# Optimization experiments

Hardware: AMD Instinct MI355X
Metric: run time of the kernel (lower is better)

Reference implementation:

```python
import jax, jax.numpy as jnp
import numpy as np

B, L, LQ = 64, 4096, 128
D = 32        # input_dim (value channels)
ET = 128      # embed_time
NH = 1        # num_heads
H = 128       # nhidden
NC = 6        # n_classes


def _time_emb(tt, lin_w, lin_b, per_w, per_b):
    # tt [..., T] -> [..., T, ET]; cat(Linear(1,1)(t), sin(Linear(1,ET-1)(t)))
    tt = tt[..., None]
    out1 = tt * lin_w[0, 0] + lin_b
    out2 = jnp.sin(tt @ per_w + per_b)
    return jnp.concatenate([out1, out2], axis=-1)


def _gru_dir(xs, wih, whh, bih, bhh, reverse):
    # xs [B, T, I] -> [B, T, H]; torch GRU gate math
    xs_t = jnp.swapaxes(xs, 0, 1)              # [T, B, I]
    if reverse:
        xs_t = xs_t[::-1]
    gi_all = xs_t @ wih.T + bih                # [T, B, 3H] precomputed input gates
    h0 = jnp.zeros((xs.shape[0], H), xs.dtype)

    def step(h, gi):
        gh = h @ whh.T + bhh
        ir, iz, inn = jnp.split(gi, 3, axis=-1)
        hr, hz, hn = jnp.split(gh, 3, axis=-1)
        r = jax.nn.sigmoid(ir + hr)
        z = jax.nn.sigmoid(iz + hz)
        n = jnp.tanh(inn + r * hn)
        h_new = (1.0 - z) * n + z * h
        return h_new, h_new

    _, ys = jax.lax.scan(step, h0, gi_all)     # [T, B, H]
    if reverse:
        ys = ys[::-1]
    return jnp.swapaxes(ys, 0, 1)


def _bigru(xs, wih, whh, bih, bhh):
    fwd = _gru_dir(xs, wih[0], whh[0], bih[0], bhh[0], False)
    bwd = _gru_dir(xs, wih[1], whh[1], bih[1], bhh[1], True)
    return jnp.concatenate([fwd, bwd], axis=-1)


def setup_inputs() -> dict:
    ks = jax.random.split(jax.random.key(0), 32)
    w = lambda i, s: jax.random.normal(ks[i], s, jnp.float32) * 0.05
    G3 = 3 * H
    return {
        "x": jax.random.normal(ks[0], (B, L, D), jnp.float32),
        "time_steps": jax.random.uniform(ks[1], (B, L), dtype=jnp.float32),
        "query_times": jnp.linspace(0.0, 1.0, LQ, dtype=jnp.float32),
        "lin_w": w(2, (1, 1)), "lin_b": w(3, (1,)),
        "per_w": w(4, (1, ET - 1)), "per_b": w(5, (ET - 1,)),
        "wq": w(6, (ET, ET)), "bq": w(7, (ET,)),
        "wk": w(8, (ET, ET)), "bk": w(9, (ET,)),
        "wo": w(10, (NH * D, H)), "bo": w(11, (H,)),
        "gru0_wih": w(12, (2, G3, H)), "gru0_whh": w(13, (2, G3, H)),
        "gru0_bih": w(14, (2, G3)), "gru0_bhh": w(15, (2, G3)),
        "gru1_wih": w(16, (2, G3, 2 * H)), "gru1_whh": w(17, (2, G3, H)),
        "gru1_bih": w(18, (2, G3)), "gru1_bhh": w(19, (2, G3)),
        "c1_w": w(20, (2 * H, 128)), "c1_b": w(21, (128,)),
        "c2_w": w(22, (128, 64)), "c2_b": w(23, (64,)),
        "c3_w": w(24, (64, NC)), "c3_b": w(25, (NC,)),
    }


def reference(x, time_steps, query_times, lin_w, lin_b, per_w, per_b,
              wq, bq, wk, bk, wo, bo,
              gru0_wih, gru0_whh, gru0_bih, gru0_bhh,
              gru1_wih, gru1_whh, gru1_bih, gru1_bhh,
              c1_w, c1_b, c2_w, c2_b, c3_w, c3_b):
    ek = ET // NH
    # learned time embeddings
    q = _time_emb(query_times[None, :], lin_w, lin_b, per_w, per_b)  # [1, LQ, ET]
    k = _time_emb(time_steps, lin_w, lin_b, per_w, per_b)            # [B, L, ET]
    # per-head projections
    qp = (q @ wq + bq).reshape(1, LQ, NH, ek).transpose(0, 2, 1, 3)[0]  # [NH, LQ, ek]
    kp = (k @ wk + bk).reshape(B, L, NH, ek).transpose(0, 2, 1, 3)      # [B, NH, L, ek]
    # mTAN attention: scores are channel-independent (mask=None), so the
    # per-channel repeat+softmax reduces to a single softmax over keys.
    scores = jnp.einsum('hqe,bhke->bhqk', qp, kp) / jnp.sqrt(jnp.float32(ek))
    p = jax.nn.softmax(scores, axis=-1)                                 # [B, NH, LQ, L]
    att = jnp.einsum('bhqk,bkd->bqhd', p, x).reshape(B, LQ, NH * D)
    att_out = att @ wo + bo                                             # [B, LQ, H]
    # 2-layer bidirectional GRU
    g0 = _bigru(att_out, gru0_wih, gru0_whh, gru0_bih, gru0_bhh)        # [B, LQ, 2H]
    g1 = _bigru(g0, gru1_wih, gru1_whh, gru1_bih, gru1_bhh)             # [B, LQ, 2H]
    class_in = jnp.concatenate([g1[:, -1, :H], g1[:, 0, H:]], axis=1)   # [B, 2H]
    out = ((class_in @ c1_w + c1_b) @ c2_w + c2_b) @ c3_w + c3_b        # [B, NC]
    return out
```

## Files before the change

### kernel.cpp

```cpp
#include <hip/hip_runtime.h>
#include <math.h>

#define Bn   64
#define Ln   4096
#define LQn  128
#define Dn   32
#define ETn  128
#define Hn   128
#define G3n  384
#define NDEG 12

typedef __attribute__((ext_vector_type(2))) float f32x2;

#define DPPF(x, ctrl) __int_as_float(__builtin_amdgcn_update_dpp(0, __float_as_int(x), (ctrl), 0xF, 0xF, true))
#define QP_XOR1 0xB1
#define QP_XOR2 0x4E
#define QP_B0   0x00
#define QP_B1   0x55
#define QP_B2   0xAA
#define QP_B3   0xFF

__device__ __forceinline__ float sin_poly(float x) {
    const float x2 = x * x;
    float r = -1.9841270114e-04f;
    r = fmaf(r, x2,  8.3333337680e-03f);
    r = fmaf(r, x2, -1.6666667163e-01f);
    return fmaf(r * x2, x, x);
}
__device__ __forceinline__ float cos_poly(float x) {
    const float x2 = x * x;
    float r =  2.4801587642e-05f;
    r = fmaf(r, x2, -1.3888888899e-03f);
    r = fmaf(r, x2,  4.1666667908e-02f);
    r = fmaf(r, x2, -5.0000000000e-01f);
    return fmaf(r, x2, 1.0f);
}

#define WS_C    0
#define WS_WT   4096
#define WS_B2   (WS_WT + 768*32)
#define WS_CLS  (WS_B2 + 1024)
#define WS_G0   (WS_CLS + Bn*2*Hn)
#define WS_GI   (WS_G0 + Bn*LQn*2*Hn)
#define WS_ACCP WS_G0
#define WS_SP   (WS_G0 + 1048576)

__global__ __launch_bounds__(128) void k_coef(
    const float* __restrict__ qtimes, const float* __restrict__ lin_w,
    const float* __restrict__ lin_b, const float* __restrict__ per_w,
    const float* __restrict__ per_b, const float* __restrict__ wq,
    const float* __restrict__ bq, const float* __restrict__ wk,
    const float* __restrict__ bk, float* __restrict__ C)
{
    __shared__ float qe[ETn], qp_l[ETn], qt_l[ETn], bas[NDEG * 128], red[96], qbk_red[32];
    const int q = blockIdx.x, tid = threadIdx.x;
    if (tid < ETn - 1) {
        const float w = per_w[tid], bb = per_b[tid];
        const float sb = sin_poly(bb), cb = cos_poly(bb);
        float wp = 1.f;
#pragma unroll
        for (int d = 0; d < NDEG; ++d) {
            const float sd = ((d & 3) == 0) ? sb : ((d & 3) == 1) ? cb : ((d & 3) == 2) ? -sb : -cb;
            bas[d * 128 + tid] = wp * sd;
            wp *= w / (float)(d + 1);
        }
    }
    const float t = qtimes[q];
    qe[tid] = (tid == 0) ? fmaf(t, lin_w[0], lin_b[0])
                         : sin_poly(fmaf(t, per_w[tid - 1], per_b[tid - 1]));
    __syncthreads();
    {
        float a = bq[tid];
#pragma unroll 16
        for (int i = 0; i < ETn; ++i) a = fmaf(qe[i], wq[i * ETn + tid], a);
        qp_l[tid] = a;
    }
    __syncthreads();
    {
        const float4* wk4 = (const float4*)(wk + (size_t)tid * ETn);
        const float4* qp4 = (const float4*)qp_l;
        float a = 0.f;
#pragma unroll
        for (int k = 0; k < 32; ++k) {
            const float4 w4 = wk4[k], p4 = qp4[k];
            a += w4.x * p4.x + w4.y * p4.y + w4.z * p4.z + w4.w * p4.w;
        }
        qt_l[tid] = a;
    }
    __syncthreads();
    if (tid < 96) {
        const int d = tid >> 3, g = tid & 7;
        float p = 0.f;
        for (int j = g; j < ETn - 1; j += 8) p = fmaf(qt_l[j + 1], bas[d * 128 + j], p);
        red[tid] = p;
    } else {
        const int g2 = tid - 96;
        float p = 0.f;
#pragma unroll
        for (int k = 0; k < 4; ++k) p = fmaf(qp_l[g2 + 32 * k], bk[g2 + 32 * k], p);
        qbk_red[g2] = p;
    }
    __syncthreads();
    if (tid < NDEG) {
        const int d = tid;
        float s = red[d * 8 + 0] + red[d * 8 + 1] + red[d * 8 + 2] + red[d * 8 + 3]
                + red[d * 8 + 4] + red[d * 8 + 5] + red[d * 8 + 6] + red[d * 8 + 7];
        if (d == 0) {
            float qbk = 0.f;
#pragma unroll
            for (int k = 0; k < 32; ++k) qbk += qbk_red[k];
            s += qt_l[0] * lin_b[0] + qbk;
        }
        if (d == 1) s += qt_l[0] * lin_w[0];
        C[q * NDEG + d] = s * 0.08838834764831845f;
    }
}

__global__ __launch_bounds__(256) void k_fuse(
    const float* __restrict__ wih, const float* __restrict__ wo,
    const float* __restrict__ bo, const float* __restrict__ bih,
    float* __restrict__ Wt, float* __restrict__ bias2)
{
    const int t = blockIdx.x * 256 + threadIdx.x;
    if (t < 768 * 32) {
        const int o = t >> 5, d = t & 31;
        const float4* wr4 = (const float4*)(wih + (size_t)o * 128);
        const float4* wc4 = (const float4*)(wo + (size_t)d * 128);
        float a = 0.f;
#pragma unroll
        for (int k = 0; k < 32; ++k) {
            const float4 r4 = wr4[k], c4 = wc4[k];
            a += r4.x * c4.x + r4.y * c4.y + r4.z * c4.z + r4.w * c4.w;
        }
        Wt[t] = a;
    } else if (t < 768 * 33) {
        const int o = t - 768 * 32;
        const float4* wr4 = (const float4*)(wih + (size_t)o * 128);
        const float4* bo4 = (const float4*)bo;
        float a = bih[o];
#pragma unroll
        for (int k = 0; k < 32; ++k) {
            const float4 r4 = wr4[k], b4 = bo4[k];
            a += r4.x * b4.x + r4.y * b4.y + r4.z * b4.z + r4.w * b4.w;
        }
        bias2[o] = a;
    }
}

__global__ __launch_bounds__(512, 1) void k_attn(
    const float* __restrict__ x, const float* __restrict__ tsteps,
    const float* __restrict__ Cc, float* __restrict__ accP, float* __restrict__ sP)
{
    __shared__ float4 xls[4 * 64 * 8];
    __shared__ float  slab[4][128][36];
    const int tid = threadIdx.x;
    const int b = blockIdx.x >> 2, lsplit = blockIdx.x & 3;
    const int i = tid & 3, qt = (tid >> 2) & 31, ls2 = tid >> 7;
    const int qown = 4 * qt + i;
    const int u = tid & 127;

    float c[NDEG];
#pragma unroll
    for (int d = 0; d < NDEG; ++d) c[d] = Cc[qown * NDEG + d];

    const int l0 = lsplit * 1024 + ls2 * 256;
    const float4* tg4 = (const float4*)(tsteps + (size_t)b * Ln + l0);
    const float4* xg  = (const float4*)(x + ((size_t)b * Ln + l0) * Dn);

    f32x2 acc2[4][4];
#pragma unroll
    for (int m = 0; m < 4; ++m)
#pragma unroll
        for (int e = 0; e < 4; ++e) { acc2[m][e].x = 0.f; acc2[m][e].y = 0.f; }
    float s_own = 0.f;

    float4 xr[4];
#pragma unroll
    for (int w = 0; w < 4; ++w) xr[w] = xg[u + 128 * w];

    for (int ch = 0; ch < 4; ++ch) {
        __syncthreads();
#pragma unroll
        for (int w = 0; w < 4; ++w) xls[ls2 * 512 + u + 128 * w] = xr[w];
        __syncthreads();
        if (ch < 3) {
            const int off = (ch + 1) * 512;
#pragma unroll
            for (int w = 0; w < 4; ++w) xr[w] = xg[off + u + 128 * w];
        }
        const float4* xrow = &xls[ls2 * 512];
        for (int k = 0; k < 16; ++k) {
            const float4 t4 = tg4[ch * 16 + k];
#pragma unroll
            for (int jj = 0; jj < 4; ++jj) {
                const float t = (jj == 0) ? t4.x : (jj == 1) ? t4.y : (jj == 2) ? t4.z : t4.w;
                float sc = c[NDEG - 1];
#pragma unroll
                for (int d = NDEG - 2; d >= 0; --d) sc = fmaf(sc, t, c[d]);
                const float pe = __expf(sc);
                s_own += pe;
                const float p0 = DPPF(pe, QP_B0);
                const float p1 = DPPF(pe, QP_B1);
                const float p2 = DPPF(pe, QP_B2);
                const float p3 = DPPF(pe, QP_B3);
                const int lrow = (k * 4 + jj) * 8;
                const float4 xa = xrow[lrow + 2 * i];
                const float4 xb = xrow[lrow + 2 * i + 1];
                f32x2 xa0; xa0.x = xa.x; xa0.y = xa.y;
                f32x2 xa1; xa1.x = xa.z; xa1.y = xa.w;
                f32x2 xb0; xb0.x = xb.x; xb0.y = xb.y;
                f32x2 xb1; xb1.x = xb.z; xb1.y = xb.w;
#define PKA(m, pv) { f32x2 pp; pp.x = (pv); pp.y = (pv); \
    acc2[m][0] = __builtin_elementwise_fma(pp, xa0, acc2[m][0]); \
    acc2[m][1] = __builtin_elementwise_fma(pp, xa1, acc2[m][1]); \
    acc2[m][2] = __builtin_elementwise_fma(pp, xb0, acc2[m][2]); \
    acc2[m][3] = __builtin_elementwise_fma(pp, xb1, acc2[m][3]); }
                PKA(0, p0) PKA(1, p1) PKA(2, p2) PKA(3, p3)
#undef PKA
            }
        }
    }
    __syncthreads();
#pragma unroll
    for (int m = 0; m < 4; ++m) {
        float4 f4a, f4b;
        f4a.x = acc2[m][0].x; f4a.y = acc2[m][0].y; f4a.z = acc2[m][1].x; f4a.w = acc2[m][1].y;
        f4b.x = acc2[m][2].x; f4b.y = acc2[m][2].y; f4b.z = acc2[m][3].x; f4b.w = acc2[m][3].y;
        *(float4*)&slab[ls2][4 * qt + m][8 * i]     = f4a;
        *(float4*)&slab[ls2][4 * qt + m][8 * i + 4] = f4b;
    }
    slab[ls2][qown][32] = s_own;
    __syncthreads();
    const int q = tid & 127, part = tid >> 7;
#pragma unroll
    for (int j = 0; j < 2; ++j) {
        const int off = (part * 2 + j) * 4;
        float4 r  = *(float4*)&slab[0][q][off];
        float4 r1 = *(float4*)&slab[1][q][off];
        float4 r2 = *(float4*)&slab[2][q][off];
        float4 r3 = *(float4*)&slab[3][q][off];
        r.x += r1.x + r2.x + r3.x; r.y += r1.y + r2.y + r3.y;
        r.z += r1.z + r2.z + r3.z; r.w += r1.w + r2.w + r3.w;
        *(float4*)&accP[((((size_t)lsplit * Bn + b) * LQn + q) * 32) + off] = r;
    }
    if (part == 0) {
        sP[((size_t)lsplit * Bn + b) * LQn + q] =
            slab[0][q][32] + slab[1][q][32] + slab[2][q][32] + slab[3][q][32];
    }
}

__global__ __launch_bounds__(256) void k_gemm_att(
    const float* __restrict__ accP, const float* __restrict__ sP,
    const float* __restrict__ Bm, const float* __restrict__ bias,
    float* __restrict__ Cm)
{
    __shared__ float4 A_l[64 * 8];
    __shared__ float4 B_l[64 * 8];
    const int tid = threadIdx.x;
    const int m0 = blockIdx.x * 64, n0 = blockIdx.y * 64;
    const int r0 = (tid >> 4) << 2, c0 = (tid & 15) << 2;
    f32x2 acc2[4][4];
#pragma unroll
    for (int a = 0; a < 4; ++a)
#pragma unroll
        for (int bb = 0; bb < 4; ++bb) { acc2[a][bb].x = 0.f; acc2[a][bb].y = 0.f; }
    const float4* Ag = (const float4*)accP;
    const float4* Bg = (const float4*)Bm;

#pragma unroll
    for (int w = 0; w < 2; ++w) {
        const int idx = tid + w * 256;
        const int row = idx >> 3, c4 = idx & 7;
        const int sc = (c4 + row + (row >> 2)) & 7;
        const int m = m0 + row;
        float4 a0 = Ag[(size_t)m * 8 + c4];
        float4 a1 = Ag[((size_t)8192  + m) * 8 + c4];
        float4 a2 = Ag[((size_t)16384 + m) * 8 + c4];
        float4 a3 = Ag[((size_t)24576 + m) * 8 + c4];
        const float inv = 1.f / (sP[m] + sP[8192 + m] + sP[16384 + m] + sP[24576 + m]);
        float4 av;
        av.x = (a0.x + a1.x + a2.x + a3.x) * inv;
        av.y = (a0.y + a1.y + a2.y + a3.y) * inv;
        av.z = (a0.z + a1.z + a2.z + a3.z) * inv;
        av.w = (a0.w + a1.w + a2.w + a3.w) * inv;
        A_l[row * 8 + sc] = av;
        B_l[row * 8 + sc] = Bg[(size_t)(n0 + row) * 8 + c4];
    }
    __syncthreads();
#pragma unroll
    for (int k4 = 0; k4 < 8; ++k4) {
        float4 av[4], bv[4];
#pragma unroll
        for (int j = 0; j < 4; ++j) {
            const int ra = r0 + j;
            av[j] = A_l[ra * 8 + ((k4 + ra + (ra >> 2)) & 7)];
        }
#pragma unroll
        for (int j = 0; j < 4; ++j) {
            const int rb = c0 + j;
            bv[j] = B_l[rb * 8 + ((k4 + rb + (rb >> 2)) & 7)];
        }
#pragma unroll
        for (int ri = 0; ri < 4; ++ri) {
            f32x2 alo; alo.x = av[ri].x; alo.y = av[ri].y;
            f32x2 ahi; ahi.x = av[ri].z; ahi.y = av[ri].w;
#pragma unroll
            for (int ci = 0; ci < 4; ++ci) {
                f32x2 blo; blo.x = bv[ci].x; blo.y = bv[ci].y;
                f32x2 bhi; bhi.x = bv[ci].z; bhi.y = bv[ci].w;
                acc2[ri][ci] = __builtin_elementwise_fma(alo, blo, acc2[ri][ci]);
                acc2[ri][ci] = __builtin_elementwise_fma(ahi, bhi, acc2[ri][ci]);
            }
        }
    }
#pragma unroll
    for (int ri = 0; ri < 4; ++ri) {
        float4 o4;
        o4.x = acc2[ri][0].x + acc2[ri][0].y + bias[n0 + c0 + 0];
        o4.y = acc2[ri][1].x + acc2[ri][1].y + bias[n0 + c0 + 1];
        o4.z = acc2[ri][2].x + acc2[ri][2].y + bias[n0 + c0 + 2];
        o4.w = acc2[ri][3].x + acc2[ri][3].y + bias[n0 + c0 + 3];
        *(float4*)&Cm[(size_t)(m0 + r0 + ri) * 768 + n0 + c0] = o4;
    }
}

__global__ __launch_bounds__(256) void k_gemm_nt(
    const float* __restrict__ A, const float* __restrict__ Bm,
    const float* __restrict__ bias, float* __restrict__ Cm,
    int N, int K)
{
    __shared__ float4 A_l[64 * 8];
    __shared__ float4 B_l[64 * 8];
    const int tid = threadIdx.x;
    const int m0 = blockIdx.x * 64, n0 = blockIdx.y * 64;
    const int r0 = (tid >> 4) << 2, c0 = (tid & 15) << 2;
    const int K4 = K >> 2;
    f32x2 acc2[4][4];
#pragma unroll
    for (int a = 0; a < 4; ++a)
#pragma unroll
        for (int bb = 0; bb < 4; ++bb) { acc2[a][bb].x = 0.f; acc2[a][bb].y = 0.f; }
    const float4* Ag = (const float4*)A;
    const float4* Bg = (const float4*)Bm;

    for (int k0 = 0; k0 < K4; k0 += 8) {
        __syncthreads();
#pragma unroll
        for (int w = 0; w < 2; ++w) {
            const int idx = tid + w * 256;
            const int row = idx >> 3, c4 = idx & 7;
            const int sc = (c4 + row + (row >> 2)) & 7;
            A_l[row * 8 + sc] = Ag[(size_t)(m0 + row) * K4 + k0 + c4];
            B_l[row * 8 + sc] = Bg[(size_t)(n0 + row) * K4 + k0 + c4];
        }
        __syncthreads();
#pragma unroll
        for (int k4 = 0; k4 < 8; ++k4) {
            float4 av[4], bv[4];
#pragma unroll
            for (int j = 0; j < 4; ++j) {
                const int ra = r0 + j;
                av[j] = A_l[ra * 8 + ((k4 + ra + (ra >> 2)) & 7)];
            }
#pragma unroll
            for (int j = 0; j < 4; ++j) {
                const int rb = c0 + j;
                bv[j] = B_l[rb * 8 + ((k4 + rb + (rb >> 2)) & 7)];
            }
#pragma unroll
            for (int ri = 0; ri < 4; ++ri) {
                f32x2 alo; alo.x = av[ri].x; alo.y = av[ri].y;
                f32x2 ahi; ahi.x = av[ri].z; ahi.y = av[ri].w;
#pragma unroll
                for (int ci = 0; ci < 4; ++ci) {
                    f32x2 blo; blo.x = bv[ci].x; blo.y = bv[ci].y;
                    f32x2 bhi; bhi.x = bv[ci].z; bhi.y = bv[ci].w;
                    acc2[ri][ci] = __builtin_elementwise_fma(alo, blo, acc2[ri][ci]);
                    acc2[ri][ci] = __builtin_elementwise_fma(ahi, bhi, acc2[ri][ci]);
                }
            }
        }
    }
#pragma unroll
    for (int ri = 0; ri < 4; ++ri) {
        float4 o4;
        o4.x = acc2[ri][0].x + acc2[ri][0].y + bias[n0 + c0 + 0];
        o4.y = acc2[ri][1].x + acc2[ri][1].y + bias[n0 + c0 + 1];
        o4.z = acc2[ri][2].x + acc2[ri][2].y + bias[n0 + c0 + 2];
        o4.w = acc2[ri][3].x + acc2[ri][3].y + bias[n0 + c0 + 3];
        *(float4*)&Cm[(size_t)(m0 + r0 + ri) * N + n0 + c0] = o4;
    }
}

__global__ __launch_bounds__(256, 1) void k_gru(
    const float* __restrict__ gi, const float* __restrict__ whh,
    const float* __restrict__ bhh, float* __restrict__ seq_out,
    float* __restrict__ final_out)
{
    __shared__ float h_l[2][Hn];
    const int tid = threadIdx.x;
    const int b = blockIdx.x >> 1, dir = blockIdx.x & 1;
    const int j = tid >> 1, q = tid & 1;

    f32x2 wr[32], wz[32], wn[32];
    {
        const float* wb = whh + ((size_t)dir * G3n + j) * Hn + 64 * q;
        const f32x2* p0 = (const f32x2*)(wb);
        const f32x2* p1 = (const f32x2*)(wb + (size_t)128 * Hn);
        const f32x2* p2 = (const f32x2*)(wb + (size_t)256 * Hn);
#pragma unroll
        for (int k = 0; k < 32; ++k) { wr[k] = p0[k]; wz[k] = p1[k]; wn[k] = p2[k]; }
    }
    const float bhr = bhh[dir * G3n + j];
    const float bhz = bhh[dir * G3n + 128 + j];
    const float bhn = bhh[dir * G3n + 256 + j];

    if (tid < Hn) { h_l[0][tid] = 0.f; h_l[1][tid] = 0.f; }
    __syncthreads();

    const long sstride = dir ? -768 : 768;
    const float* gptr = gi + (size_t)b * LQn * 768 + dir * G3n + j
                        + (size_t)(dir ? LQn - 1 : 0) * 768;

    int cur = 0;
    float hlast = 0.f;

    auto gstep = [&](const float gir, const float giz, const float gin,
                     const int step) {
        const float hold = h_l[cur][j];
        const float4* hb = (const float4*)(&h_l[cur][q * 64]);
        f32x2 ar = {0.f, 0.f}, az = {0.f, 0.f}, an = {0.f, 0.f};
        f32x2 br = {0.f, 0.f}, bz = {0.f, 0.f}, bn = {0.f, 0.f};
#pragma unroll
        for (int cc = 0; cc < 16; ++cc) {
            float4 hv = hb[cc];
            f32x2 h01; h01.x = hv.x; h01.y = hv.y;
            f32x2 h23; h23.x = hv.z; h23.y = hv.w;
            asm("v_pk_fma_f32 %0, %1, %2, %0" : "+v"(ar) : "v"(wr[2 * cc]),     "v"(h01));
            asm("v_pk_fma_f32 %0, %1, %2, %0" : "+v"(az) : "v"(wz[2 * cc]),     "v"(h01));
            asm("v_pk_fma_f32 %0, %1, %2, %0" : "+v"(an) : "v"(wn[2 * cc]),     "v"(h01));
            asm("v_pk_fma_f32 %0, %1, %2, %0" : "+v"(br) : "v"(wr[2 * cc + 1]), "v"(h23));
            asm("v_pk_fma_f32 %0, %1, %2, %0" : "+v"(bz) : "v"(wz[2 * cc + 1]), "v"(h23));
            asm("v_pk_fma_f32 %0, %1, %2, %0" : "+v"(bn) : "v"(wn[2 * cc + 1]), "v"(h23));
        }
        float sr = (ar.x + br.x) + (ar.y + br.y);
        float sz = (az.x + bz.x) + (az.y + bz.y);
        float sn = (an.x + bn.x) + (an.y + bn.y);
        sr += DPPF(sr, QP_XOR1);
        sz += DPPF(sz, QP_XOR1);
        sn += DPPF(sn, QP_XOR1);
        const float r = 1.f / (1.f + __expf(-(gir + sr + bhr)));
        const float z = 1.f / (1.f + __expf(-(giz + sz + bhz)));
        const float nx = gin + r * (sn + bhn);
        const float n = 1.f - 2.f / (1.f + __expf(2.f * nx));
        const float hn = n + z * (hold - n);
        if (q == 0) {
            h_l[cur ^ 1][j] = hn;
            if (seq_out) {
                const int l = dir ? (LQn - 1 - step) : step;
                seq_out[((size_t)(b * LQn + l)) * (2 * Hn) + dir * Hn + j] = hn;
            }
        }
        hlast = hn;
        cur ^= 1;
        __syncthreads();
    };

    float gA[3], gB[3], gC[3], gD[3];
#define GLD(dst, s) { const long o = (long)(s) * sstride; \
    dst[0] = gptr[o]; dst[1] = gptr[o + 128]; dst[2] = gptr[o + 256]; }
    GLD(gA, 0) GLD(gB, 1) GLD(gC, 2) GLD(gD, 3)
    for (int s0 = 0; s0 < LQn; s0 += 4) {
        gstep(gA[0], gA[1], gA[2], s0);
        { const int sn2 = (s0 + 4 < LQn) ? s0 + 4 : LQn - 1; GLD(gA, sn2) }
        gstep(gB[0], gB[1], gB[2], s0 + 1);
        { const int sn2 = (s0 + 5 < LQn) ? s0 + 5 : LQn - 1; GLD(gB, sn2) }
        gstep(gC[0], gC[1], gC[2], s0 + 2);
        { const int sn2 = (s0 + 6 < LQn) ? s0 + 6 : LQn - 1; GLD(gC, sn2) }
        gstep(gD[0], gD[1], gD[2], s0 + 3);
        { const int sn2 = (s0 + 7 < LQn) ? s0 + 7 : LQn - 1; GLD(gD, sn2) }
    }
#undef GLD
    if (final_out && q == 0) final_out[b * 2 * Hn + dir * Hn + j] = hlast;
}

__global__ __launch_bounds__(256) void k_cls(
    const float* __restrict__ cls_in,
    const float* __restrict__ c1w, const float* __restrict__ c1b,
    const float* __restrict__ c2w, const float* __restrict__ c2b,
    const float* __restrict__ c3w, const float* __restrict__ c3b,
    float* __restrict__ out)
{
    __shared__ float ci[256], y1[128], y2[64];
    const int b = blockIdx.x, tid = threadIdx.x;
    ci[tid] = cls_in[b * 256 + tid];
    __syncthreads();
    if (tid < 128) { float a = c1b[tid]; for (int i = 0; i < 256; ++i) a += ci[i] * c1w[i * 128 + tid]; y1[tid] = a; }
    __syncthreads();
    if (tid < 64)  { float a = c2b[tid]; for (int i = 0; i < 128; ++i) a += y1[i] * c2w[i * 64 + tid];  y2[tid] = a; }
    __syncthreads();
    if (tid < 6)   { float a = c3b[tid]; for (int i = 0; i < 64; ++i)  a += y2[i] * c3w[i * 6 + tid];   out[b * 6 + tid] = a; }
}

extern "C" void kernel_launch(void* const* d_in, const int* in_sizes, int n_in,
                              void* d_out, int out_size, void* d_ws, size_t ws_size,
                              hipStream_t stream)
{
    const float* x        = (const float*)d_in[0];
    const float* tsteps   = (const float*)d_in[1];
    const float* qtimes   = (const float*)d_in[2];
    const float* lin_w    = (const float*)d_in[3];
    const float* lin_b    = (const float*)d_in[4];
    const float* per_w    = (const float*)d_in[5];
    const float* per_b    = (const float*)d_in[6];
    const float* wq       = (const float*)d_in[7];
    const float* bq       = (const float*)d_in[8];
    const float* wk       = (const float*)d_in[9];
    const float* bk       = (const float*)d_in[10];
    const float* wo       = (const float*)d_in[11];
    const float* bo       = (const float*)d_in[12];
    const float* g0_wih   = (const float*)d_in[13];
    const float* g0_whh   = (const float*)d_in[14];
    const float* g0_bih   = (const float*)d_in[15];
    const float* g0_bhh   = (const float*)d_in[16];
    const float* g1_wih   = (const float*)d_in[17];
    const float* g1_whh   = (const float*)d_in[18];
    const float* g1_bih   = (const float*)d_in[19];
    const float* g1_bhh   = (const float*)d_in[20];
    const float* c1w      = (const float*)d_in[21];
    const float* c1b      = (const float*)d_in[22];
    const float* c2w      = (const float*)d_in[23];
    const float* c2b      = (const float*)d_in[24];
    const float* c3w      = (const float*)d_in[25];
    const float* c3b      = (const float*)d_in[26];
    float* out = (float*)d_out;
    float* ws  = (float*)d_ws;

    float* Cws   = ws + WS_C;
    float* Wt    = ws + WS_WT;
    float* bias2 = ws + WS_B2;
    float* clsin = ws + WS_CLS;
    float* g0buf = ws + WS_G0;
    float* accP  = ws + WS_ACCP;
    float* sPb   = ws + WS_SP;
    float* gibuf = ws + WS_GI;

    k_coef<<<128, 128, 0, stream>>>(qtimes, lin_w, lin_b, per_w, per_b, wq, bq, wk, bk, Cws);
    k_fuse<<<99, 256, 0, stream>>>(g0_wih, wo, bo, g0_bih, Wt, bias2);
    k_attn<<<256, 512, 0, stream>>>(x, tsteps, Cws, accP, sPb);

    k_gemm_att<<<dim3(128, 12), 256, 0, stream>>>(accP, sPb, Wt, bias2, gibuf);
    k_gru<<<128, 256, 0, stream>>>(gibuf, g0_whh, g0_bhh, g0buf, nullptr);

    k_gemm_nt<<<dim3(128, 12), 256, 0, stream>>>(g0buf, g1_wih, g1_bih, gibuf, 768, 256);
    k_gru<<<128, 256, 0, stream>>>(gibuf, g1_whh, g1_bhh, nullptr, clsin);

    k_cls<<<64, 256, 0, stream>>>(clsin, c1w, c1b, c2w, c2b, c3w, c3b, out);
}
```

Measured before the change: 325.2 us.

## Use fp16 dot2 recurrent matvec in GRU with 4 lanes per hidden unit

The GRU recurrent weights are converted to fp16 and kept in registers, and the hidden state is mirrored in fp16 in shared memory so that v_dot2_f32_f16 can replace packed fp32 FMAs. The block doubles to 512 threads with 4 lanes per hidden unit, which halves the per-thread dot length and uses a two-stage DPP reduction. Each lane loads one of the three input-gate values, and these are spread across the quad with DPP broadcasts. This targets the serial per-step latency of the recurrence. The cost is reduced precision in the recurrent matvec, which can accumulate over 128 steps, plus a larger barrier across 8 waves.

```diff
diff --git a/kernel.cpp b/kernel.cpp
--- a/kernel.cpp
+++ b/kernel.cpp
@@ -11,6 +11,7 @@
 #define NDEG 12
 
 typedef __attribute__((ext_vector_type(2))) float f32x2;
+typedef __attribute__((ext_vector_type(2))) _Float16 f16x2;
 
 #define DPPF(x, ctrl) __int_as_float(__builtin_amdgcn_update_dpp(0, __float_as_int(x), (ctrl), 0xF, 0xF, true))
 #define QP_XOR1 0xB1
@@ -392,96 +393,117 @@
     }
 }
 
-__global__ __launch_bounds__(256, 1) void k_gru(
+__global__ __launch_bounds__(512) void k_gru(
     const float* __restrict__ gi, const float* __restrict__ whh,
     const float* __restrict__ bhh, float* __restrict__ seq_out,
     float* __restrict__ final_out)
 {
-    __shared__ float h_l[2][Hn];
+    __shared__ _Float16 h16[2][Hn];
+    __shared__ float    h32[2][Hn];
     const int tid = threadIdx.x;
     const int b = blockIdx.x >> 1, dir = blockIdx.x & 1;
-    const int j = tid >> 1, q = tid & 1;
-
-    f32x2 wr[32], wz[32], wn[32];
+    const int j = tid >> 2, q = tid & 3;
+
+    f16x2 wr[16], wz[16], wn[16];
     {
-        const float* wb = whh + ((size_t)dir * G3n + j) * Hn + 64 * q;
+        const float* wb = whh + ((size_t)dir * G3n + j) * Hn + 32 * q;
         const f32x2* p0 = (const f32x2*)(wb);
         const f32x2* p1 = (const f32x2*)(wb + (size_t)128 * Hn);
         const f32x2* p2 = (const f32x2*)(wb + (size_t)256 * Hn);
 #pragma unroll
-        for (int k = 0; k < 32; ++k) { wr[k] = p0[k]; wz[k] = p1[k]; wn[k] = p2[k]; }
+        for (int k = 0; k < 16; ++k) {
+            f32x2 a = p0[k], bz2 = p1[k], c2 = p2[k];
+            wr[k].x = (_Float16)a.x;   wr[k].y = (_Float16)a.y;
+            wz[k].x = (_Float16)bz2.x; wz[k].y = (_Float16)bz2.y;
+            wn[k].x = (_Float16)c2.x;  wn[k].y = (_Float16)c2.y;
+        }
+    }
+#pragma unroll
+    for (int k = 0; k < 16; ++k) {
+        asm volatile("" : "+v"(wr[k]));
+        asm volatile("" : "+v"(wz[k]));
+        asm volatile("" : "+v"(wn[k]));
     }
     const float bhr = bhh[dir * G3n + j];
     const float bhz = bhh[dir * G3n + 128 + j];
     const float bhn = bhh[dir * G3n + 256 + j];
 
-    if (tid < Hn) { h_l[0][tid] = 0.f; h_l[1][tid] = 0.f; }
+    if (tid < 2 * Hn) { ((_Float16*)h16)[tid] = (_Float16)0.f; ((float*)h32)[tid] = 0.f; }
     __syncthreads();
 
     const long sstride = dir ? -768 : 768;
-    const float* gptr = gi + (size_t)b * LQn * 768 + dir * G3n + j
+    const float* gptr = gi + (size_t)b * LQn * 768 + dir * G3n + q * Hn + j
                         + (size_t)(dir ? LQn - 1 : 0) * 768;
+    const bool ldq = (q < 3);
 
     int cur = 0;
     float hlast = 0.f;
 
-    auto gstep = [&](const float gir, const float giz, const float gin,
-                     const int step) {
-        const float hold = h_l[cur][j];
-        const float4* hb = (const float4*)(&h_l[cur][q * 64]);
-        f32x2 ar = {0.f, 0.f}, az = {0.f, 0.f}, an = {0.f, 0.f};
-        f32x2 br = {0.f, 0.f}, bz = {0.f, 0.f}, bn = {0.f, 0.f};
-#pragma unroll
-        for (int cc = 0; cc < 16; ++cc) {
-            float4 hv = hb[cc];
-            f32x2 h01; h01.x = hv.x; h01.y = hv.y;
-            f32x2 h23; h23.x = hv.z; h23.y = hv.w;
-            asm("v_pk_fma_f32 %0, %1, %2, %0" : "+v"(ar) : "v"(wr[2 * cc]),     "v"(h01));
-            asm("v_pk_fma_f32 %0, %1, %2, %0" : "+v"(az) : "v"(wz[2 * cc]),     "v"(h01));
-            asm("v_pk_fma_f32 %0, %1, %2, %0" : "+v"(an) : "v"(wn[2 * cc]),     "v"(h01));
-            asm("v_pk_fma_f32 %0, %1, %2, %0" : "+v"(br) : "v"(wr[2 * cc + 1]), "v"(h23));
-            asm("v_pk_fma_f32 %0, %1, %2, %0" : "+v"(bz) : "v"(wz[2 * cc + 1]), "v"(h23));
-            asm("v_pk_fma_f32 %0, %1, %2, %0" : "+v"(bn) : "v"(wn[2 * cc + 1]), "v"(h23));
-        }
-        float sr = (ar.x + br.x) + (ar.y + br.y);
-        float sz = (az.x + bz.x) + (az.y + bz.y);
-        float sn = (an.x + bn.x) + (an.y + bn.y);
-        sr += DPPF(sr, QP_XOR1);
-        sz += DPPF(sz, QP_XOR1);
-        sn += DPPF(sn, QP_XOR1);
+    auto gstep = [&](const float gi_cur, const int step) {
+        const float hold = h32[cur][j];
+        const float4* hb4 = (const float4*)(&h16[cur][32 * q]);
+        float sr = 0.f, sz = 0.f, sn = 0.f;
+#pragma unroll
+        for (int k2 = 0; k2 < 4; ++k2) {
+            float4 hv = hb4[k2];
+            f16x2 h0 = *(f16x2*)&hv.x;
+            f16x2 h1 = *(f16x2*)&hv.y;
+            f16x2 h2 = *(f16x2*)&hv.z;
+            f16x2 h3 = *(f16x2*)&hv.w;
+            asm("v_dot2_f32_f16 %0, %1, %2, %0" : "+v"(sr) : "v"(wr[4 * k2 + 0]), "v"(h0));
+            asm("v_dot2_f32_f16 %0, %1, %2, %0" : "+v"(sz) : "v"(wz[4 * k2 + 0]), "v"(h0));
+            asm("v_dot2_f32_f16 %0, %1, %2, %0" : "+v"(sn) : "v"(wn[4 * k2 + 0]), "v"(h0));
+            asm("v_dot2_f32_f16 %0, %1, %2, %0" : "+v"(sr) : "v"(wr[4 * k2 + 1]), "v"(h1));
+            asm("v_dot2_f32_f16 %0, %1, %2, %0" : "+v"(sz) : "v"(wz[4 * k2 + 1]), "v"(h1));
+            asm("v_dot2_f32_f16 %0, %1, %2, %0" : "+v"(sn) : "v"(wn[4 * k2 + 1]), "v"(h1));
+            asm("v_dot2_f32_f16 %0, %1, %2, %0" : "+v"(sr) : "v"(wr[4 * k2 + 2]), "v"(h2));
+            asm("v_dot2_f32_f16 %0, %1, %2, %0" : "+v"(sz) : "v"(wz[4 * k2 + 2]), "v"(h2));
+            asm("v_dot2_f32_f16 %0, %1, %2, %0" : "+v"(sn) : "v"(wn[4 * k2 + 2]), "v"(h2));
+            asm("v_dot2_f32_f16 %0, %1, %2, %0" : "+v"(sr) : "v"(wr[4 * k2 + 3]), "v"(h3));
+            asm("v_dot2_f32_f16 %0, %1, %2, %0" : "+v"(sz) : "v"(wz[4 * k2 + 3]), "v"(h3));
+            asm("v_dot2_f32_f16 %0, %1, %2, %0" : "+v"(sn) : "v"(wn[4 * k2 + 3]), "v"(h3));
+        }
+        sr += DPPF(sr, QP_XOR1); sr += DPPF(sr, QP_XOR2);
+        sz += DPPF(sz, QP_XOR1); sz += DPPF(sz, QP_XOR2);
+        sn += DPPF(sn, QP_XOR1); sn += DPPF(sn, QP_XOR2);
+        const float gir = DPPF(gi_cur, QP_B0);
+        const float giz = DPPF(gi_cur, QP_B1);
+        const float gin = DPPF(gi_cur, QP_B2);
         const float r = 1.f / (1.f + __expf(-(gir + sr + bhr)));
         const float z = 1.f / (1.f + __expf(-(giz + sz + bhz)));
         const float nx = gin + r * (sn + bhn);
         const float n = 1.f - 2.f / (1.f + __expf(2.f * nx));
         const float hn = n + z * (hold - n);
         if (q == 0) {
-            h_l[cur ^ 1][j] = hn;
+            h32[cur ^ 1][j] = hn;
+            h16[cur ^ 1][j] = (_Float16)hn;
+        }
+        if (q == 3) {
             if (seq_out) {
                 const int l = dir ? (LQn - 1 - step) : step;
                 seq_out[((size_t)(b * LQn + l)) * (2 * Hn) + dir * Hn + j] = hn;
             }
-        }
-        hlast = hn;
+            hlast = hn;
+        }
         cur ^= 1;
-        __syncthreads();
+        asm volatile("s_waitcnt lgkmcnt(0)\n\ts_barrier" ::: "memory");
     };
 
-    float gA[3], gB[3], gC[3], gD[3];
-#define GLD(dst, s) { const long o = (long)(s) * sstride; \
-    dst[0] = gptr[o]; dst[1] = gptr[o + 128]; dst[2] = gptr[o + 256]; }
+    float gA, gB, gC, gD;
+#define GLD(d, s) { d = ldq ? gptr[(long)(s) * sstride] : 0.f; }
     GLD(gA, 0) GLD(gB, 1) GLD(gC, 2) GLD(gD, 3)
     for (int s0 = 0; s0 < LQn; s0 += 4) {
-        gstep(gA[0], gA[1], gA[2], s0);
+        gstep(gA, s0);
         { const int sn2 = (s0 + 4 < LQn) ? s0 + 4 : LQn - 1; GLD(gA, sn2) }
-        gstep(gB[0], gB[1], gB[2], s0 + 1);
+        gstep(gB, s0 + 1);
         { const int sn2 = (s0 + 5 < LQn) ? s0 + 5 : LQn - 1; GLD(gB, sn2) }
-        gstep(gC[0], gC[1], gC[2], s0 + 2);
+        gstep(gC, s0 + 2);
         { const int sn2 = (s0 + 6 < LQn) ? s0 + 6 : LQn - 1; GLD(gC, sn2) }
-        gstep(gD[0], gD[1], gD[2], s0 + 3);
+        gstep(gD, s0 + 3);
         { const int sn2 = (s0 + 7 < LQn) ? s0 + 7 : LQn - 1; GLD(gD, sn2) }
     }
 #undef GLD
-    if (final_out && q == 0) final_out[b * 2 * Hn + dir * Hn + j] = hlast;
+    if (final_out && q == 3) final_out[b * 2 * Hn + dir * Hn + j] = hlast;
 }
 
 __global__ __launch_bounds__(256) void k_cls(
@@ -550,10 +572,10 @@
     k_attn<<<256, 512, 0, stream>>>(x, tsteps, Cws, accP, sPb);
 
     k_gemm_att<<<dim3(128, 12), 256, 0, stream>>>(accP, sPb, Wt, bias2, gibuf);
-    k_gru<<<128, 256, 0, stream>>>(gibuf, g0_whh, g0_bhh, g0buf, nullptr);
+    k_gru<<<128, 512, 0, stream>>>(gibuf, g0_whh, g0_bhh, g0buf, nullptr);
 
     k_gemm_nt<<<dim3(128, 12), 256, 0, stream>>>(g0buf, g1_wih, g1_bih, gibuf, 768, 256);
-    k_gru<<<128, 256, 0, stream>>>(gibuf, g1_whh, g1_bhh, nullptr, clsin);
+    k_gru<<<128, 512, 0, stream>>>(gibuf, g1_whh, g1_bhh, nullptr, clsin);
 
     k_cls<<<64, 256, 0, stream>>>(clsin, c1w, c1b, c2w, c2b, c3w, c3b, out);
 }
```

After: 332.1 us. 1.02x slower.
